# Kernel optimization log

Hardware: AMD Instinct MI355X
Metric: run time of the kernel (lower is better)

## Reference

```python
import jax, jax.numpy as jnp
import numpy as np

B, T, C, H = 4, 2048, 1024, 16
HD = C // H  # head_dim = 64


def setup_inputs() -> dict:
    key = jax.random.key(0)
    k1, k2, k3, k4, k5 = jax.random.split(key, 5)
    s = 1.0 / np.sqrt(C)
    return {
        "x": jax.random.normal(k1, (B, T, C), dtype=jnp.float32),
        "W_attn": jax.random.normal(k2, (C, 3 * C), dtype=jnp.float32) * s,
        "b_attn": jax.random.normal(k3, (3 * C,), dtype=jnp.float32) * 0.02,
        "W_proj": jax.random.normal(k4, (C, C), dtype=jnp.float32) * s,
        "b_proj": jax.random.normal(k5, (C,), dtype=jnp.float32) * 0.02,
    }


def reference(x, W_attn, b_attn, W_proj, b_proj):
    b, t, c = x.shape
    qkv = x @ W_attn + b_attn                      # [B,T,3C]
    q, k, v = jnp.split(qkv, 3, axis=-1)
    # [B,T,C] -> [B,H,T,HD]
    q = q.reshape(b, t, H, HD).transpose(0, 2, 1, 3)
    k = k.reshape(b, t, H, HD).transpose(0, 2, 1, 3)
    v = v.reshape(b, t, H, HD).transpose(0, 2, 1, 3)
    att = jnp.einsum("bhqd,bhkd->bhqk", q, k) * (1.0 / np.sqrt(HD))
    causal = jnp.tril(jnp.ones((t, t), dtype=bool))
    att = jnp.where(causal[None, None], att, -jnp.inf)
    att = jax.nn.softmax(att, axis=-1)
    y = jnp.einsum("bhqk,bhkd->bhqd", att, v)      # [B,H,T,HD]
    y = y.transpose(0, 2, 1, 3).reshape(b, t, c)
    return y @ W_proj + b_proj
```

## Files before the change

kernel.cpp:

```cpp
#include <hip/hip_runtime.h>
#include <hip/hip_bf16.h>

#define B_ 4
#define T_ 2048
#define C_ 1024
#define H_ 16
#define HD_ 64
#define M_ (B_*T_)
#define N3_ (3*C_)
#define QKVSZ (B_*H_*T_*HD_)
#define QSCALE 0.1803368801f

typedef unsigned short u16;
typedef unsigned int u32;
typedef __attribute__((ext_vector_type(8))) __bf16 bf16x8;
typedef __attribute__((ext_vector_type(4))) float f32x4;
typedef __attribute__((ext_vector_type(16))) float f32x16;
typedef __attribute__((ext_vector_type(2))) int i32x2;
typedef __attribute__((ext_vector_type(4))) u32 u32x4;
typedef const __attribute__((address_space(1))) void* gptr_t;
typedef __attribute__((address_space(3))) void* sptr_t;

__device__ __forceinline__ u16 f2b(float f) {
  __hip_bfloat16 h = __float2bfloat16(f);
  return __builtin_bit_cast(u16, h);
}

__device__ __forceinline__ u32 cvtpk(float lo, float hi) {
  u32 r;
  asm volatile("v_cvt_pk_bf16_f32 %0, %1, %2" : "=v"(r) : "v"(lo), "v"(hi));
  return r;
}

__global__ __launch_bounds__(256) void cvt_kernel(const float* __restrict__ src,
                                                  u16* __restrict__ dst, int n4) {
  int i = blockIdx.x * blockDim.x + threadIdx.x;
  int stride = gridDim.x * blockDim.x;
  for (; i < n4; i += stride) {
    float4 f = ((const float4*)src)[i];
    ushort4 o;
    o.x = f2b(f.x); o.y = f2b(f.y); o.z = f2b(f.z); o.w = f2b(f.w);
    ((ushort4*)dst)[i] = o;
  }
}

__global__ __launch_bounds__(256) void tr_cvt2(const float* __restrict__ Wa,
                                               u16* __restrict__ Wat,
                                               const float* __restrict__ Wp,
                                               u16* __restrict__ Wpt) {
  __shared__ u16 tile[64][72];
  const bool attn = (blockIdx.y < 48);
  const float* src = attn ? Wa : Wp;
  u16* dst = attn ? Wat : Wpt;
  const int N = attn ? N3_ : C_;
  int k0 = blockIdx.x * 64, n0 = (attn ? blockIdx.y : blockIdx.y - 48) * 64;
  #pragma unroll
  for (int t = 0; t < 16; ++t) {
    int idx = threadIdx.x + t * 256;
    int r = idx >> 6, c = idx & 63;
    tile[r][c] = f2b(src[(size_t)(k0 + r) * N + n0 + c]);
  }
  __syncthreads();
  #pragma unroll
  for (int t = 0; t < 16; ++t) {
    int idx = threadIdx.x + t * 256;
    int r = idx >> 6, c = idx & 63;
    dst[(size_t)(n0 + r) * C_ + k0 + c] = tile[c][r];
  }
}

template <int EPI>
__global__ __launch_bounds__(256, 2) void gemm_bt(const u16* __restrict__ A,
                                                  const u16* __restrict__ Bt,
                                                  const float* __restrict__ bias,
                                                  int K, int N,
                                                  u16* __restrict__ out_qkv,
                                                  float* __restrict__ out_f) {
  __shared__ __align__(16) u16 As[2][128 * 64];
  __shared__ __align__(16) u16 Bs[2][128 * 64];
  const int tid = threadIdx.x;
  const int wave = tid >> 6, lane = tid & 63;
  const int lr = lane & 15, lk = lane >> 4;

  const int m0 = blockIdx.x * 128, n0 = blockIdx.y * 128;
  const int wr = (wave >> 1) * 64, wc = (wave & 1) * 64;

  f32x4 acc[4][4] = {};

  auto stage = [&](int buf, int it) {
    const int kt = it * 64;
    #pragma unroll
    for (int i = 0; i < 4; ++i) {
      int ch = i * 256 + tid;
      int row = ch >> 3;
      int gsrc = (ch & 7) ^ (row & 7);
      __builtin_amdgcn_global_load_lds((gptr_t)(A + (size_t)(m0 + row) * K + kt + gsrc * 8),
                                       (sptr_t)(&As[buf][ch * 8]), 16, 0, 0);
    }
    #pragma unroll
    for (int i = 0; i < 4; ++i) {
      int ch = i * 256 + tid;
      int row = ch >> 3;
      int gsrc = (ch & 7) ^ (row & 7);
      __builtin_amdgcn_global_load_lds((gptr_t)(Bt + (size_t)(n0 + row) * K + kt + gsrc * 8),
                                       (sptr_t)(&Bs[buf][ch * 8]), 16, 0, 0);
    }
  };

  const int KI = K / 64;
  stage(0, 0);
  asm volatile("s_waitcnt vmcnt(0)" ::: "memory");
  __builtin_amdgcn_s_barrier();

  for (int it = 0; it < KI; ++it) {
    const int cur = it & 1;
    if (it + 1 < KI) stage(cur ^ 1, it + 1);

    #pragma unroll
    for (int h = 0; h < 2; ++h) {
      bf16x8 af[4], bfr[4];
      #pragma unroll
      for (int mi = 0; mi < 4; ++mi) {
        int r = wr + mi * 16 + lr;
        af[mi] = *(const bf16x8*)(&As[cur][r * 64 + (((4 * h + lk) ^ (r & 7)) << 3)]);
      }
      #pragma unroll
      for (int ni = 0; ni < 4; ++ni) {
        int r = wc + ni * 16 + lr;
        bfr[ni] = *(const bf16x8*)(&Bs[cur][r * 64 + (((4 * h + lk) ^ (r & 7)) << 3)]);
      }
      __builtin_amdgcn_s_setprio(1);
      #pragma unroll
      for (int mi = 0; mi < 4; ++mi)
        #pragma unroll
        for (int ni = 0; ni < 4; ++ni)
          acc[mi][ni] = __builtin_amdgcn_mfma_f32_16x16x32_bf16(af[mi], bfr[ni], acc[mi][ni], 0, 0, 0);
      __builtin_amdgcn_s_setprio(0);
    }

    asm volatile("s_waitcnt vmcnt(0)" ::: "memory");
    __builtin_amdgcn_s_barrier();
  }

  if (EPI == 0) {
    const int sel = (n0 >> 10);
    #pragma unroll
    for (int mi = 0; mi < 4; ++mi) {
      #pragma unroll
      for (int ni = 0; ni < 4; ++ni) {
        int m = m0 + wr + mi * 16 + lk * 4;
        int n = n0 + wc + ni * 16 + lr;
        int rem = n & 1023, h = rem >> 6, d = rem & 63;
        int b = m >> 11, t = m & 2047;
        if (sel == 2) {
          ushort4 st;
          #pragma unroll
          for (int j = 0; j < 4; ++j)
            ((u16*)&st)[j] = f2b(acc[mi][ni][j] + bias[n]);
          *(ushort4*)(out_qkv + 2 * (size_t)QKVSZ +
                      (((size_t)(b * H_ + h) * HD_ + d) * T_ + t)) = st;
        } else {
          #pragma unroll
          for (int j = 0; j < 4; ++j) {
            float val = acc[mi][ni][j] + bias[n];
            if (sel == 0) val *= QSCALE;
            out_qkv[(size_t)sel * QKVSZ +
                    (((size_t)(b * H_ + h) * T_ + (t + j)) * HD_ + d)] = f2b(val);
          }
        }
      }
    }
  } else {
    #pragma unroll
    for (int mi = 0; mi < 4; ++mi)
      #pragma unroll
      for (int ni = 0; ni < 4; ++ni)
        #pragma unroll
        for (int j = 0; j < 4; ++j) {
          int m = m0 + wr + mi * 16 + lk * 4 + j;
          int n = n0 + wc + ni * 16 + lr;
          out_f[(size_t)m * C_ + n] = acc[mi][ni][j] + bias[n];
        }
  }
}

__global__ __launch_bounds__(256, 4) void attn_k(const u16* __restrict__ q,
                                                 const u16* __restrict__ k,
                                                 const u16* __restrict__ vt,
                                                 u16* __restrict__ y) {
  __shared__ __align__(16) u16 Ks[2][64 * 64];
  __shared__ __align__(16) u16 Vs[2][64 * 64];
  const int tid = threadIdx.x;
  const int wave = tid >> 6, lane = tid & 63;
  const int hi = lane >> 5, lq = lane & 31;
  const int qtb = gridDim.y - 1 - blockIdx.y;
  const int bh = blockIdx.x;
  const size_t koff = (size_t)bh * T_ * HD_;
  const size_t voff = (size_t)bh * HD_ * T_;
  const int qrow = qtb * 128 + 32 * wave + lq;
  const int sw = (lq & 7) ^ ((lq >> 3) & 3);

  bf16x8 qf[4];
  #pragma unroll
  for (int c = 0; c < 4; ++c)
    qf[c] = *(const bf16x8*)(q + koff + (size_t)qrow * HD_ + 16 * c + 8 * hi);

  f32x16 o[2] = {};
  float mrun = -1e30f, lsum = 0.f;

  auto stage = [&](int buf, int kt) {
    const u16* kb = k + koff + (size_t)kt * 64 * HD_;
    const u16* vb = vt + voff + (size_t)kt * 64;
    #pragma unroll
    for (int j = 0; j < 2; ++j) {
      int cb = j * 256 + wave * 64;
      int ch = cb + lane;
      int row = ch >> 3, gg = ch & 7;
      int src = gg ^ (row & 7) ^ ((row >> 3) & 3);
      __builtin_amdgcn_global_load_lds((gptr_t)(kb + row * HD_ + src * 8),
                                       (sptr_t)(&Ks[buf][cb * 8]), 16, 0, 0);
      __builtin_amdgcn_global_load_lds((gptr_t)(vb + (size_t)row * T_ + src * 8),
                                       (sptr_t)(&Vs[buf][cb * 8]), 16, 0, 0);
    }
  };

  const int nt = 2 * qtb + 2;
  stage(0, 0);
  __syncthreads();

  for (int kt = 0; kt < nt; ++kt) {
    const int cur = kt & 1;
    if (kt + 1 < nt) stage(cur ^ 1, kt + 1);
    const bool active = (kt <= 2 * qtb + (wave >> 1));
    if (active) {
      const bool dia = (kt == 2 * qtb + (wave >> 1));
      const bool skip1 = dia && ((wave & 1) == 0);
      const u16* Kb = &Ks[cur][0];
      const u16* Vb = &Vs[cur][0];

      f32x16 s[2] = {};
      __builtin_amdgcn_s_setprio(1);
      #pragma unroll
      for (int c = 0; c < 4; ++c) {
        #pragma unroll
        for (int kh = 0; kh < 2; ++kh) {
          if (kh == 1 && skip1) continue;
          int row = 32 * kh + lq;
          bf16x8 kf = *(const bf16x8*)(Kb + row * 64 + (((2 * c + hi) ^ sw) << 3));
          s[kh] = __builtin_amdgcn_mfma_f32_32x32x16_bf16(kf, qf[c], s[kh], 0, 0, 0);
        }
      }
      __builtin_amdgcn_s_setprio(0);

      if (dia) {
        #pragma unroll
        for (int rr = 0; rr < 16; ++rr) {
          int kg = 64 * kt + 4 * hi + (rr & 3) + 8 * (rr >> 2);
          if ((wave & 1) == 0) { if (kg > qrow)      s[0][rr] = -1e30f; }
          else                 { if (kg + 32 > qrow) s[1][rr] = -1e30f; }
        }
      }

      float g0, g1, g2, g3;
      {
        const f32x16& a = s[0];
        g0 = fmaxf(fmaxf(a[0], a[1]),   fmaxf(a[2], a[3]));
        g1 = fmaxf(fmaxf(a[4], a[5]),   fmaxf(a[6], a[7]));
        g2 = fmaxf(fmaxf(a[8], a[9]),   fmaxf(a[10], a[11]));
        g3 = fmaxf(fmaxf(a[12], a[13]), fmaxf(a[14], a[15]));
      }
      if (!skip1) {
        const f32x16& a = s[1];
        g0 = fmaxf(g0, fmaxf(fmaxf(a[0], a[1]),   fmaxf(a[2], a[3])));
        g1 = fmaxf(g1, fmaxf(fmaxf(a[4], a[5]),   fmaxf(a[6], a[7])));
        g2 = fmaxf(g2, fmaxf(fmaxf(a[8], a[9]),   fmaxf(a[10], a[11])));
        g3 = fmaxf(g3, fmaxf(fmaxf(a[12], a[13]), fmaxf(a[14], a[15])));
      }
      float tm = fmaxf(fmaxf(g0, g1), fmaxf(g2, g3));
      tm = fmaxf(tm, __shfl_xor(tm, 32));
      if (__any(tm > mrun + 8.f)) {
        float mn = fmaxf(mrun, tm);
        float al = __builtin_amdgcn_exp2f(mrun - mn);
        lsum *= al;
        o[0] *= al;
        o[1] *= al;
        mrun = mn;
      }
      float rs = 0.f;
      #pragma unroll
      for (int kh = 0; kh < 2; ++kh) {
        if (kh == 1 && skip1) continue;
        #pragma unroll
        for (int rr = 0; rr < 16; ++rr) {
          float p = __builtin_amdgcn_exp2f(s[kh][rr] - mrun);
          s[kh][rr] = p;
          rs += p;
        }
      }
      rs += __shfl_xor(rs, 32);
      lsum += rs;

      #pragma unroll
      for (int kh = 0; kh < 2; ++kh) {
        if (kh == 1 && skip1) continue;
        bf16x8 pf[2];
        #pragma unroll
        for (int ct = 0; ct < 2; ++ct) {
          u32 A0 = cvtpk(s[kh][8 * ct + 0], s[kh][8 * ct + 1]);
          u32 A1 = cvtpk(s[kh][8 * ct + 2], s[kh][8 * ct + 3]);
          u32 B0 = cvtpk(s[kh][8 * ct + 4], s[kh][8 * ct + 5]);
          u32 B1 = cvtpk(s[kh][8 * ct + 6], s[kh][8 * ct + 7]);
          i32x2 r0 = __builtin_amdgcn_permlane32_swap((int)A0, (int)B0, false, false);
          i32x2 r1 = __builtin_amdgcn_permlane32_swap((int)A1, (int)B1, false, false);
          u32x4 w = {(u32)r0[0], (u32)r1[0], (u32)r0[1], (u32)r1[1]};
          pf[ct] = __builtin_bit_cast(bf16x8, w);
        }
        __builtin_amdgcn_s_setprio(1);
        #pragma unroll
        for (int ct = 0; ct < 2; ++ct)
          #pragma unroll
          for (int dh = 0; dh < 2; ++dh) {
            int row = 32 * dh + lq;
            bf16x8 vf = *(const bf16x8*)(Vb + row * 64 + (((4 * kh + 2 * ct + hi) ^ sw) << 3));
            o[dh] = __builtin_amdgcn_mfma_f32_32x32x16_bf16(vf, pf[ct], o[dh], 0, 0, 0);
          }
        __builtin_amdgcn_s_setprio(0);
      }
    }
    __syncthreads();
  }

  const int b = bh >> 4, h = bh & 15;
  float li = 1.0f / lsum;
  u16* yrow = y + (size_t)(b * T_ + qrow) * C_ + h * 64;
  #pragma unroll
  for (int dh = 0; dh < 2; ++dh)
    #pragma unroll
    for (int u = 0; u < 4; ++u) {
      ushort4 st;
      st.x = f2b(o[dh][4 * u + 0] * li);
      st.y = f2b(o[dh][4 * u + 1] * li);
      st.z = f2b(o[dh][4 * u + 2] * li);
      st.w = f2b(o[dh][4 * u + 3] * li);
      *(ushort4*)(yrow + 32 * dh + 8 * u + 4 * hi) = st;
    }
}

extern "C" void kernel_launch(void* const* d_in, const int* in_sizes, int n_in,
                              void* d_out, int out_size, void* d_ws, size_t ws_size,
                              hipStream_t stream) {
  const float* x      = (const float*)d_in[0];
  const float* W_attn = (const float*)d_in[1];
  const float* b_attn = (const float*)d_in[2];
  const float* W_proj = (const float*)d_in[3];
  const float* b_proj = (const float*)d_in[4];
  float* out = (float*)d_out;

  u16* ws = (u16*)d_ws;
  u16* xb  = ws;
  u16* Wat = xb + (size_t)M_ * C_;
  u16* Wpt = Wat + (size_t)N3_ * C_;
  u16* qkv = Wpt + (size_t)C_ * C_;
  u16* y   = qkv + (size_t)3 * QKVSZ;

  cvt_kernel<<<2048, 256, 0, stream>>>(x, xb, M_ * C_ / 4);
  tr_cvt2<<<dim3(C_ / 64, 64), 256, 0, stream>>>(W_attn, Wat, W_proj, Wpt);
  gemm_bt<0><<<dim3(M_ / 128, N3_ / 128), 256, 0, stream>>>(xb, Wat, b_attn, C_, N3_, qkv, nullptr);
  attn_k<<<dim3(B_ * H_, T_ / 128), 256, 0, stream>>>(qkv, qkv + QKVSZ, qkv + 2 * QKVSZ, y);
  gemm_bt<1><<<dim3(M_ / 128, C_ / 128), 256, 0, stream>>>(y, Wpt, b_proj, C_, C_, nullptr, out);
}
```

Before: 166.4 us.

## Process 64 query rows per wave with 2 waves per attention block

Restructures the attention kernel so each wave handles two 32-row query sub-tiles (64 rows) and each block uses 2 waves instead of 4. Each K/V fragment read from LDS now feeds two MFMAs, halving LDS reads per unit of compute. The cost is about twice the registers per wave (two sets of accumulators and softmax state) and fewer waves per block to hide latency. The diagonal-tile skip of the masked half is dropped, so some fully masked MFMA work is now computed.

```diff
diff --git a/kernel.cpp b/kernel.cpp
--- a/kernel.cpp
+++ b/kernel.cpp
@@ -184,7 +184,7 @@
   }
 }
 
-__global__ __launch_bounds__(256, 4) void attn_k(const u16* __restrict__ q,
+__global__ __launch_bounds__(128, 2) void attn_k(const u16* __restrict__ q,
                                                  const u16* __restrict__ k,
                                                  const u16* __restrict__ vt,
                                                  u16* __restrict__ y) {
@@ -197,23 +197,26 @@
   const int bh = blockIdx.x;
   const size_t koff = (size_t)bh * T_ * HD_;
   const size_t voff = (size_t)bh * HD_ * T_;
-  const int qrow = qtb * 128 + 32 * wave + lq;
+  const int qrow = qtb * 128 + 64 * wave + lq;
   const int sw = (lq & 7) ^ ((lq >> 3) & 3);
 
-  bf16x8 qf[4];
+  bf16x8 qf[2][4];
   #pragma unroll
-  for (int c = 0; c < 4; ++c)
-    qf[c] = *(const bf16x8*)(q + koff + (size_t)qrow * HD_ + 16 * c + 8 * hi);
-
-  f32x16 o[2] = {};
-  float mrun = -1e30f, lsum = 0.f;
+  for (int qs = 0; qs < 2; ++qs)
+    #pragma unroll
+    for (int c = 0; c < 4; ++c)
+      qf[qs][c] = *(const bf16x8*)(q + koff + (size_t)(qrow + 32 * qs) * HD_ + 16 * c + 8 * hi);
+
+  f32x16 o[2][2] = {};
+  float mrun[2] = {-1e30f, -1e30f};
+  float lsum[2] = {0.f, 0.f};
 
   auto stage = [&](int buf, int kt) {
     const u16* kb = k + koff + (size_t)kt * 64 * HD_;
     const u16* vb = vt + voff + (size_t)kt * 64;
     #pragma unroll
-    for (int j = 0; j < 2; ++j) {
-      int cb = j * 256 + wave * 64;
+    for (int j = 0; j < 4; ++j) {
+      int cb = j * 128 + wave * 64;
       int ch = cb + lane;
       int row = ch >> 3, gg = ch & 7;
       int src = gg ^ (row & 7) ^ ((row >> 3) & 3);
@@ -231,90 +234,94 @@
   for (int kt = 0; kt < nt; ++kt) {
     const int cur = kt & 1;
     if (kt + 1 < nt) stage(cur ^ 1, kt + 1);
-    const bool active = (kt <= 2 * qtb + (wave >> 1));
+    const bool active = (kt <= 2 * qtb + wave);
     if (active) {
-      const bool dia = (kt == 2 * qtb + (wave >> 1));
-      const bool skip1 = dia && ((wave & 1) == 0);
+      const bool dia = (kt == 2 * qtb + wave);
       const u16* Kb = &Ks[cur][0];
       const u16* Vb = &Vs[cur][0];
 
-      f32x16 s[2] = {};
+      f32x16 s[2][2] = {};
       __builtin_amdgcn_s_setprio(1);
       #pragma unroll
       for (int c = 0; c < 4; ++c) {
         #pragma unroll
         for (int kh = 0; kh < 2; ++kh) {
-          if (kh == 1 && skip1) continue;
           int row = 32 * kh + lq;
           bf16x8 kf = *(const bf16x8*)(Kb + row * 64 + (((2 * c + hi) ^ sw) << 3));
-          s[kh] = __builtin_amdgcn_mfma_f32_32x32x16_bf16(kf, qf[c], s[kh], 0, 0, 0);
+          s[kh][0] = __builtin_amdgcn_mfma_f32_32x32x16_bf16(kf, qf[0][c], s[kh][0], 0, 0, 0);
+          s[kh][1] = __builtin_amdgcn_mfma_f32_32x32x16_bf16(kf, qf[1][c], s[kh][1], 0, 0, 0);
         }
       }
       __builtin_amdgcn_s_setprio(0);
 
       if (dia) {
         #pragma unroll
+        for (int qs = 0; qs < 2; ++qs) {
+          int qg = qrow + 32 * qs;
+          #pragma unroll
+          for (int rr = 0; rr < 16; ++rr) {
+            int kg = 64 * kt + 4 * hi + (rr & 3) + 8 * (rr >> 2);
+            if (kg > qg)      s[0][qs][rr] = -1e30f;
+            if (kg + 32 > qg) s[1][qs][rr] = -1e30f;
+          }
+        }
+      }
+
+      #pragma unroll
+      for (int qs = 0; qs < 2; ++qs) {
+        const f32x16& a = s[0][qs];
+        const f32x16& bq = s[1][qs];
+        float g0 = fmaxf(fmaxf(fmaxf(a[0], a[1]),   fmaxf(a[2], a[3])),
+                         fmaxf(fmaxf(bq[0], bq[1]), fmaxf(bq[2], bq[3])));
+        float g1 = fmaxf(fmaxf(fmaxf(a[4], a[5]),   fmaxf(a[6], a[7])),
+                         fmaxf(fmaxf(bq[4], bq[5]), fmaxf(bq[6], bq[7])));
+        float g2 = fmaxf(fmaxf(fmaxf(a[8], a[9]),   fmaxf(a[10], a[11])),
+                         fmaxf(fmaxf(bq[8], bq[9]), fmaxf(bq[10], bq[11])));
+        float g3 = fmaxf(fmaxf(fmaxf(a[12], a[13]), fmaxf(a[14], a[15])),
+                         fmaxf(fmaxf(bq[12], bq[13]), fmaxf(bq[14], bq[15])));
+        float tm = fmaxf(fmaxf(g0, g1), fmaxf(g2, g3));
+        tm = fmaxf(tm, __shfl_xor(tm, 32));
+        if (__any(tm > mrun[qs] + 8.f)) {
+          float mn = fmaxf(mrun[qs], tm);
+          float al = __builtin_amdgcn_exp2f(mrun[qs] - mn);
+          lsum[qs] *= al;
+          o[qs][0] *= al;
+          o[qs][1] *= al;
+          mrun[qs] = mn;
+        }
+        float p0[16], p1[16];
+        #pragma unroll
         for (int rr = 0; rr < 16; ++rr) {
-          int kg = 64 * kt + 4 * hi + (rr & 3) + 8 * (rr >> 2);
-          if ((wave & 1) == 0) { if (kg > qrow)      s[0][rr] = -1e30f; }
-          else                 { if (kg + 32 > qrow) s[1][rr] = -1e30f; }
-        }
-      }
-
-      float g0, g1, g2, g3;
-      {
-        const f32x16& a = s[0];
-        g0 = fmaxf(fmaxf(a[0], a[1]),   fmaxf(a[2], a[3]));
-        g1 = fmaxf(fmaxf(a[4], a[5]),   fmaxf(a[6], a[7]));
-        g2 = fmaxf(fmaxf(a[8], a[9]),   fmaxf(a[10], a[11]));
-        g3 = fmaxf(fmaxf(a[12], a[13]), fmaxf(a[14], a[15]));
-      }
-      if (!skip1) {
-        const f32x16& a = s[1];
-        g0 = fmaxf(g0, fmaxf(fmaxf(a[0], a[1]),   fmaxf(a[2], a[3])));
-        g1 = fmaxf(g1, fmaxf(fmaxf(a[4], a[5]),   fmaxf(a[6], a[7])));
-        g2 = fmaxf(g2, fmaxf(fmaxf(a[8], a[9]),   fmaxf(a[10], a[11])));
-        g3 = fmaxf(g3, fmaxf(fmaxf(a[12], a[13]), fmaxf(a[14], a[15])));
-      }
-      float tm = fmaxf(fmaxf(g0, g1), fmaxf(g2, g3));
-      tm = fmaxf(tm, __shfl_xor(tm, 32));
-      if (__any(tm > mrun + 8.f)) {
-        float mn = fmaxf(mrun, tm);
-        float al = __builtin_amdgcn_exp2f(mrun - mn);
-        lsum *= al;
-        o[0] *= al;
-        o[1] *= al;
-        mrun = mn;
-      }
-      float rs = 0.f;
+          p0[rr] = __builtin_amdgcn_exp2f(s[0][qs][rr] - mrun[qs]);
+          p1[rr] = __builtin_amdgcn_exp2f(s[1][qs][rr] - mrun[qs]);
+          s[0][qs][rr] = p0[rr];
+          s[1][qs][rr] = p1[rr];
+        }
+        float t0 = ((p0[0] + p0[1]) + (p0[2] + p0[3])) + ((p0[4] + p0[5]) + (p0[6] + p0[7]));
+        float t1 = ((p0[8] + p0[9]) + (p0[10] + p0[11])) + ((p0[12] + p0[13]) + (p0[14] + p0[15]));
+        float t2 = ((p1[0] + p1[1]) + (p1[2] + p1[3])) + ((p1[4] + p1[5]) + (p1[6] + p1[7]));
+        float t3 = ((p1[8] + p1[9]) + (p1[10] + p1[11])) + ((p1[12] + p1[13]) + (p1[14] + p1[15]));
+        float rs = (t0 + t1) + (t2 + t3);
+        rs += __shfl_xor(rs, 32);
+        lsum[qs] += rs;
+      }
+
       #pragma unroll
       for (int kh = 0; kh < 2; ++kh) {
-        if (kh == 1 && skip1) continue;
-        #pragma unroll
-        for (int rr = 0; rr < 16; ++rr) {
-          float p = __builtin_amdgcn_exp2f(s[kh][rr] - mrun);
-          s[kh][rr] = p;
-          rs += p;
-        }
-      }
-      rs += __shfl_xor(rs, 32);
-      lsum += rs;
-
-      #pragma unroll
-      for (int kh = 0; kh < 2; ++kh) {
-        if (kh == 1 && skip1) continue;
-        bf16x8 pf[2];
-        #pragma unroll
-        for (int ct = 0; ct < 2; ++ct) {
-          u32 A0 = cvtpk(s[kh][8 * ct + 0], s[kh][8 * ct + 1]);
-          u32 A1 = cvtpk(s[kh][8 * ct + 2], s[kh][8 * ct + 3]);
-          u32 B0 = cvtpk(s[kh][8 * ct + 4], s[kh][8 * ct + 5]);
-          u32 B1 = cvtpk(s[kh][8 * ct + 6], s[kh][8 * ct + 7]);
-          i32x2 r0 = __builtin_amdgcn_permlane32_swap((int)A0, (int)B0, false, false);
-          i32x2 r1 = __builtin_amdgcn_permlane32_swap((int)A1, (int)B1, false, false);
-          u32x4 w = {(u32)r0[0], (u32)r1[0], (u32)r0[1], (u32)r1[1]};
-          pf[ct] = __builtin_bit_cast(bf16x8, w);
-        }
+        bf16x8 pf[2][2];
+        #pragma unroll
+        for (int qs = 0; qs < 2; ++qs)
+          #pragma unroll
+          for (int ct = 0; ct < 2; ++ct) {
+            u32 A0 = cvtpk(s[kh][qs][8 * ct + 0], s[kh][qs][8 * ct + 1]);
+            u32 A1 = cvtpk(s[kh][qs][8 * ct + 2], s[kh][qs][8 * ct + 3]);
+            u32 B0 = cvtpk(s[kh][qs][8 * ct + 4], s[kh][qs][8 * ct + 5]);
+            u32 B1 = cvtpk(s[kh][qs][8 * ct + 6], s[kh][qs][8 * ct + 7]);
+            i32x2 r0 = __builtin_amdgcn_permlane32_swap((int)A0, (int)B0, false, false);
+            i32x2 r1 = __builtin_amdgcn_permlane32_swap((int)A1, (int)B1, false, false);
+            u32x4 w = {(u32)r0[0], (u32)r1[0], (u32)r0[1], (u32)r1[1]};
+            pf[qs][ct] = __builtin_bit_cast(bf16x8, w);
+          }
         __builtin_amdgcn_s_setprio(1);
         #pragma unroll
         for (int ct = 0; ct < 2; ++ct)
@@ -322,7 +329,8 @@
           for (int dh = 0; dh < 2; ++dh) {
             int row = 32 * dh + lq;
             bf16x8 vf = *(const bf16x8*)(Vb + row * 64 + (((4 * kh + 2 * ct + hi) ^ sw) << 3));
-            o[dh] = __builtin_amdgcn_mfma_f32_32x32x16_bf16(vf, pf[ct], o[dh], 0, 0, 0);
+            o[0][dh] = __builtin_amdgcn_mfma_f32_32x32x16_bf16(vf, pf[0][ct], o[0][dh], 0, 0, 0);
+            o[1][dh] = __builtin_amdgcn_mfma_f32_32x32x16_bf16(vf, pf[1][ct], o[1][dh], 0, 0, 0);
           }
         __builtin_amdgcn_s_setprio(0);
       }
@@ -331,19 +339,23 @@
   }
 
   const int b = bh >> 4, h = bh & 15;
-  float li = 1.0f / lsum;
-  u16* yrow = y + (size_t)(b * T_ + qrow) * C_ + h * 64;
   #pragma unroll
-  for (int dh = 0; dh < 2; ++dh)
-    #pragma unroll
-    for (int u = 0; u < 4; ++u) {
-      ushort4 st;
-      st.x = f2b(o[dh][4 * u + 0] * li);
-      st.y = f2b(o[dh][4 * u + 1] * li);
-      st.z = f2b(o[dh][4 * u + 2] * li);
-      st.w = f2b(o[dh][4 * u + 3] * li);
-      *(ushort4*)(yrow + 32 * dh + 8 * u + 4 * hi) = st;
-    }
+  for (int qs = 0; qs < 2; ++qs) {
+    float li = 1.0f / lsum[qs];
+    int t = qrow + 32 * qs;
+    u16* yrow = y + (size_t)(b * T_ + t) * C_ + h * 64;
+    #pragma unroll
+    for (int dh = 0; dh < 2; ++dh)
+      #pragma unroll
+      for (int u = 0; u < 4; ++u) {
+        ushort4 st;
+        st.x = f2b(o[qs][dh][4 * u + 0] * li);
+        st.y = f2b(o[qs][dh][4 * u + 1] * li);
+        st.z = f2b(o[qs][dh][4 * u + 2] * li);
+        st.w = f2b(o[qs][dh][4 * u + 3] * li);
+        *(ushort4*)(yrow + 32 * dh + 8 * u + 4 * hi) = st;
+      }
+  }
 }
 
 extern "C" void kernel_launch(void* const* d_in, const int* in_sizes, int n_in,
@@ -366,6 +378,6 @@
   cvt_kernel<<<2048, 256, 0, stream>>>(x, xb, M_ * C_ / 4);
   tr_cvt2<<<dim3(C_ / 64, 64), 256, 0, stream>>>(W_attn, Wat, W_proj, Wpt);
   gemm_bt<0><<<dim3(M_ / 128, N3_ / 128), 256, 0, stream>>>(xb, Wat, b_attn, C_, N3_, qkv, nullptr);
-  attn_k<<<dim3(B_ * H_, T_ / 128), 256, 0, stream>>>(qkv, qkv + QKVSZ, qkv + 2 * QKVSZ, y);
+  attn_k<<<dim3(B_ * H_, T_ / 128), 128, 0, stream>>>(qkv, qkv + QKVSZ, qkv + 2 * QKVSZ, y);
   gemm_bt<1><<<dim3(M_ / 128, C_ / 128), 256, 0, stream>>>(y, Wpt, b_proj, C_, C_, nullptr, out);
 }
```

New measurement: 180.6 us. 8.5% more time.
